# Optimization experiments

Measured on AMD Instinct MI355X. Metric: run time of the kernel, lower is better.

Reference implementation:

```python
import jax, jax.numpy as jnp
import numpy as np

N = 100_000      # nodes
E = 3_200_000    # directed edges
F_IN = 128       # node feature dim
H = 16           # hidden channels


def setup_inputs() -> dict:
    key = jax.random.key(0)
    k0, k1, k2, k3, k4, k5 = jax.random.split(key, 6)
    x = jax.random.normal(k0, (N, F_IN), dtype=jnp.float32)
    edge_index = jax.random.randint(k1, (2, E), 0, N, dtype=jnp.int32)
    W1 = jax.random.normal(k2, (F_IN, H), dtype=jnp.float32) * (1.0 / np.sqrt(F_IN))
    b1 = jax.random.normal(k3, (H,), dtype=jnp.float32) * 0.02
    W2 = jax.random.normal(k4, (H, 1), dtype=jnp.float32) * (1.0 / np.sqrt(H))
    b2 = jax.random.normal(k5, (1,), dtype=jnp.float32) * 0.02
    return {"x": x, "edge_index": edge_index, "W1": W1, "b1": b1, "W2": W2, "b2": b2}


def _gcn_conv(x, src, dst, deg_inv_sqrt, W, b):
    # PyG GCNConv: h = x @ W; out_i = sum_{j->i} norm_ij * h_j + b
    # norm_ij = deg_i^-1/2 * deg_j^-1/2 (degrees include self-loops)
    n = x.shape[0]
    h = x @ W                                   # [N, out]
    norm = deg_inv_sqrt[src] * deg_inv_sqrt[dst]  # [E+N]
    msg = h[src] * norm[:, None]                # gather + scale
    out = jax.ops.segment_sum(msg, dst, num_segments=n)
    return out + b


def reference(x, edge_index, W1, b1, W2, b2):
    n = x.shape[0]
    loops = jnp.arange(n, dtype=edge_index.dtype)
    src = jnp.concatenate([edge_index[0], loops])  # self-loops appended
    dst = jnp.concatenate([edge_index[1], loops])
    # degree of destination nodes (with self-loops), shared by both layers
    deg = jax.ops.segment_sum(jnp.ones_like(dst, dtype=x.dtype), dst, num_segments=n)
    deg_inv_sqrt = jax.lax.rsqrt(jnp.maximum(deg, 1.0))  # deg >= 1 due to self-loops

    h = jax.nn.relu(_gcn_conv(x, src, dst, deg_inv_sqrt, W1, b1))
    out = _gcn_conv(h, src, dst, deg_inv_sqrt, W2, b2)
    return out
```

## Files before the change

kernel.cpp:

```cpp
#include <hip/hip_runtime.h>
#include <hip/hip_fp16.h>

#define FIN 128
#define HC 16
#define NBLK 512
#define NB 391
#define BKT 256
#define SLOT 17408
#define SENT 0xFFFFFFFFu
#define SMAX 5

typedef _Float16 half8 __attribute__((ext_vector_type(8)));
typedef float f32x4 __attribute__((ext_vector_type(4)));

__global__ __launch_bounds__(1024) void count_kernel(const int* __restrict__ dst,
                                                     int* __restrict__ cntTab, int E) {
    __shared__ int cnt[NB];
    int blk = blockIdx.x, t = threadIdx.x;
    for (int i = t; i < NB; i += 1024) cnt[i] = 0;
    __syncthreads();
    int slice = (((E + NBLK - 1) / NBLK) + 3) & ~3;
    int s = blk * slice, e = min(E, s + slice);
    if (s < e) {
        int n4 = (e - s) >> 2;
        const int4* d4 = (const int4*)(dst + s);
        for (int i = t; i < n4; i += 1024) {
            int4 dd = d4[i];
            atomicAdd(&cnt[dd.x >> 8], 1);
            atomicAdd(&cnt[dd.y >> 8], 1);
            atomicAdd(&cnt[dd.z >> 8], 1);
            atomicAdd(&cnt[dd.w >> 8], 1);
        }
    }
    __syncthreads();
    for (int i = t; i < NB; i += 1024) cntTab[i * NBLK + blk] = cnt[i];
}

__global__ void rowscan_kernel(const int* __restrict__ cntTab, int* __restrict__ rowEx,
                               int* __restrict__ bucketTotal) {
    __shared__ int wsum[8];
    int b = blockIdx.x, t = threadIdx.x;
    int own = cntTab[b * NBLK + t];
    int rnd = (own + 15) & ~15;
    int sc = rnd;
#pragma unroll
    for (int off = 1; off < 64; off <<= 1) {
        int v = __shfl_up(sc, off);
        if ((t & 63) >= off) sc += v;
    }
    if ((t & 63) == 63) wsum[t >> 6] = sc;
    __syncthreads();
    int pre = 0;
#pragma unroll
    for (int w = 0; w < 8; ++w)
        if (w < (t >> 6)) pre += wsum[w];
    int inc = sc + pre;
    rowEx[b * NBLK + t] = inc - rnd;
    if (t == NBLK - 1) bucketTotal[b] = inc;
}

__global__ __launch_bounds__(1024) void scatter_kernel(const int* __restrict__ src,
                                                       const int* __restrict__ dst,
                                                       const int* __restrict__ rowEx,
                                                       unsigned int* __restrict__ ebuf, int E) {
    __shared__ int base[NB];
    __shared__ int cur[NB];
    int blk = blockIdx.x, t = threadIdx.x;
    for (int i = t; i < NB; i += 1024) {
        base[i] = i * SLOT + rowEx[i * NBLK + blk];
        cur[i] = 0;
    }
    __syncthreads();
    int slice = (((E + NBLK - 1) / NBLK) + 3) & ~3;
    int s = blk * slice, e = min(E, s + slice);
    if (s < e) {
        int n4 = (e - s) >> 2;
        const int4* d4 = (const int4*)(dst + s);
        const int4* s4 = (const int4*)(src + s);
        for (int i = t; i < n4; i += 1024) {
            int4 dd = d4[i];
            int4 ss = s4[i];
            int b0 = dd.x >> 8, p0 = atomicAdd(&cur[b0], 1);
            ebuf[base[b0] + p0] = ((unsigned)ss.x << 8) | (unsigned)(dd.x & 255);
            int b1 = dd.y >> 8, p1 = atomicAdd(&cur[b1], 1);
            ebuf[base[b1] + p1] = ((unsigned)ss.y << 8) | (unsigned)(dd.y & 255);
            int b2 = dd.z >> 8, p2 = atomicAdd(&cur[b2], 1);
            ebuf[base[b2] + p2] = ((unsigned)ss.z << 8) | (unsigned)(dd.z & 255);
            int b3 = dd.w >> 8, p3 = atomicAdd(&cur[b3], 1);
            ebuf[base[b3] + p3] = ((unsigned)ss.w << 8) | (unsigned)(dd.w & 255);
        }
    }
    __syncthreads();
    for (int i = t; i < NB; i += 1024) {
        int c = cur[i], r = (c + 15) & ~15;
        int bb = base[i];
        for (int p = c; p < r; ++p) ebuf[bb + p] = SENT;
    }
}

__global__ __launch_bounds__(1024) void sortdis_kernel(const unsigned int* __restrict__ ebuf,
                                                       const int* __restrict__ bucketTotal,
                                                       int* __restrict__ csr, int* __restrict__ offs,
                                                       int* __restrict__ deg, float* __restrict__ dis,
                                                       int n) {
    __shared__ int cnt[BKT];
    __shared__ int sc[BKT];
    int b = blockIdx.x, t = threadIdx.x;
    if (t < BKT) cnt[t] = 0;
    __syncthreads();
    int s0 = b * SLOT;
    int total = bucketTotal[b];
    int n4 = total >> 2;
    const uint4* e4 = (const uint4*)(ebuf + s0);
    uint4 ent[SMAX];
    int rk[SMAX][4];
#pragma unroll
    for (int j = 0; j < SMAX; ++j) {
        int idx = j * 1024 + t;
        if (idx < n4) {
            uint4 u = e4[idx];
            ent[j] = u;
            rk[j][0] = (u.x != SENT) ? atomicAdd(&cnt[u.x & 255], 1) : -1;
            rk[j][1] = (u.y != SENT) ? atomicAdd(&cnt[u.y & 255], 1) : -1;
            rk[j][2] = (u.z != SENT) ? atomicAdd(&cnt[u.z & 255], 1) : -1;
            rk[j][3] = (u.w != SENT) ? atomicAdd(&cnt[u.w & 255], 1) : -1;
        } else {
            ent[j].x = SENT; ent[j].y = SENT; ent[j].z = SENT; ent[j].w = SENT;
            rk[j][0] = rk[j][1] = rk[j][2] = rk[j][3] = -1;
        }
    }
    __syncthreads();
    if (t < 64) {
        int c0 = cnt[t * 4], c1 = cnt[t * 4 + 1], c2 = cnt[t * 4 + 2], c3 = cnt[t * 4 + 3];
        int s = c0 + c1 + c2 + c3;
        int scv = s;
#pragma unroll
        for (int off = 1; off < 64; off <<= 1) {
            int v = __shfl_up(scv, off);
            if (t >= off) scv += v;
        }
        int base = scv - s;
        sc[t * 4] = base;
        sc[t * 4 + 1] = base + c0;
        sc[t * 4 + 2] = base + c0 + c1;
        sc[t * 4 + 3] = base + c0 + c1 + c2;
    }
    __syncthreads();
    if (t < BKT) {
        int node = b * BKT + t;
        if (node < n) {
            offs[node] = s0 + sc[t];
            deg[node] = cnt[t];
            dis[node] = rsqrtf((float)cnt[t] + 1.0f);
        }
    }
#pragma unroll
    for (int j = 0; j < SMAX; ++j) {
        unsigned ux = ent[j].x;
        if (ux != SENT) csr[s0 + sc[ux & 255] + rk[j][0]] = (int)(ux >> 8);
        unsigned uy = ent[j].y;
        if (uy != SENT) csr[s0 + sc[uy & 255] + rk[j][1]] = (int)(uy >> 8);
        unsigned uz = ent[j].z;
        if (uz != SENT) csr[s0 + sc[uz & 255] + rk[j][2]] = (int)(uz >> 8);
        unsigned uw = ent[j].w;
        if (uw != SENT) csr[s0 + sc[uw & 255] + rk[j][3]] = (int)(uw >> 8);
    }
}

__global__ void h1_mfma_kernel(const float* __restrict__ x, const float* __restrict__ W1,
                               const float* __restrict__ dis, __half* __restrict__ hs16, int n) {
    __shared__ float xs[64][132];
    int t = threadIdx.x;
    int wave = t >> 6;
    int lane = t & 63;
    int r = lane & 15, g = lane >> 4;
    int rowbase0 = blockIdx.x * 64;
#pragma unroll
    for (int it = 0; it < 8; ++it) {
        int i = it * 256 + t;
        int row = i >> 5, c4 = i & 31;
        int grow = rowbase0 + row;
        const float4* xr = (const float4*)(x + (size_t)(grow < n ? grow : n - 1) * FIN);
        float4 v = xr[c4];
        xs[row][c4 * 4 + 0] = v.x;
        xs[row][c4 * 4 + 1] = v.y;
        xs[row][c4 * 4 + 2] = v.z;
        xs[row][c4 * 4 + 3] = v.w;
    }
    half8 bfrag[4];
#pragma unroll
    for (int i = 0; i < 4; ++i)
#pragma unroll
        for (int j = 0; j < 8; ++j)
            bfrag[i][j] = (_Float16)W1[(i * 32 + g * 8 + j) * HC + r];
    __syncthreads();
    int rowbase = wave * 16;
    f32x4 acc = {0.f, 0.f, 0.f, 0.f};
#pragma unroll
    for (int i = 0; i < 4; ++i) {
        const float4* rowp = (const float4*)&xs[rowbase + r][i * 32 + g * 8];
        float4 v0 = rowp[0];
        float4 v1 = rowp[1];
        half8 afrag;
        afrag[0] = (_Float16)v0.x; afrag[1] = (_Float16)v0.y;
        afrag[2] = (_Float16)v0.z; afrag[3] = (_Float16)v0.w;
        afrag[4] = (_Float16)v1.x; afrag[5] = (_Float16)v1.y;
        afrag[6] = (_Float16)v1.z; afrag[7] = (_Float16)v1.w;
        acc = __builtin_amdgcn_mfma_f32_16x16x32_f16(afrag, bfrag[i], acc, 0, 0, 0);
    }
#pragma unroll
    for (int j = 0; j < 4; ++j) {
        int orow = rowbase0 + rowbase + g * 4 + j;
        if (orow < n) hs16[(size_t)orow * HC + r] = __float2half(acc[j] * dis[orow]);
    }
}

__global__ void pull_layer1_kernel(const int* __restrict__ offs, const int* __restrict__ deg,
                                   const int* __restrict__ csr,
                                   const __half2* __restrict__ hs16, const float* __restrict__ dis,
                                   const float* __restrict__ b1, const float* __restrict__ W2,
                                   float* __restrict__ h2s, int n) {
    int node = (blockIdx.x * blockDim.x + threadIdx.x) >> 6;
    if (node >= n) return;
    int lane = threadIdx.x & 63;
    int cp = lane & 7;
    int eg = lane >> 3;
    int start = offs[node];
    int m = deg[node];
    int sidx = (lane < m) ? csr[start + lane] : 0;
    int mm = min(m, 64);
    float ax = 0.f, ay = 0.f;
    if (mm <= 32) {
#pragma unroll
        for (int t = 0; t < 4; ++t) {
            int e = t * 8 + eg;
            int s = __shfl(sidx, e);
            float2 f = __half22float2(hs16[(size_t)s * 8 + cp]);
            if (e < mm) { ax += f.x; ay += f.y; }
        }
    } else {
#pragma unroll
        for (int t = 0; t < 8; ++t) {
            int e = t * 8 + eg;
            int s = __shfl(sidx, e);
            float2 f = __half22float2(hs16[(size_t)s * 8 + cp]);
            if (e < mm) { ax += f.x; ay += f.y; }
        }
        for (int k = 64 + eg; k < m; k += 8) {
            float2 f = __half22float2(hs16[(size_t)csr[start + k] * 8 + cp]);
            ax += f.x; ay += f.y;
        }
    }
    ax += __shfl_xor(ax, 8);  ay += __shfl_xor(ay, 8);
    ax += __shfl_xor(ax, 16); ay += __shfl_xor(ay, 16);
    ax += __shfl_xor(ax, 32); ay += __shfl_xor(ay, 32);
    float d = dis[node];
    float2 self = __half22float2(hs16[(size_t)node * 8 + cp]);
    float h1a = fmaxf(fmaf(d, ax + self.x, b1[2 * cp]), 0.f);
    float h1b = fmaxf(fmaf(d, ay + self.y, b1[2 * cp + 1]), 0.f);
    float v = h1a * W2[2 * cp] + h1b * W2[2 * cp + 1];
    v += __shfl_xor(v, 1);
    v += __shfl_xor(v, 2);
    v += __shfl_xor(v, 4);
    if (lane == 0) h2s[node] = v * d;
}

__global__ void pull_layer2_kernel(const int* __restrict__ offs, const int* __restrict__ deg,
                                   const int* __restrict__ csr,
                                   const float* __restrict__ h2s, const float* __restrict__ dis,
                                   const float* __restrict__ b2, float* __restrict__ out, int n) {
    int g = blockIdx.x * blockDim.x + threadIdx.x;
    int node = g >> 3;
    if (node >= n) return;
    int q = g & 7;
    int start = offs[node];
    int m = deg[node];
    float a = 0.f;
    int k = q;
    for (; k + 24 < m; k += 32) {
        int i0 = csr[start + k];
        int i1 = csr[start + k + 8];
        int i2 = csr[start + k + 16];
        int i3 = csr[start + k + 24];
        float g0 = h2s[i0], g1 = h2s[i1], g2 = h2s[i2], g3 = h2s[i3];
        a += (g0 + g1) + (g2 + g3);
    }
    for (; k < m; k += 8) a += h2s[csr[start + k]];
    a += __shfl_xor(a, 1);
    a += __shfl_xor(a, 2);
    a += __shfl_xor(a, 4);
    if (q == 0) out[node] = dis[node] * (a + h2s[node]) + b2[0];
}

extern "C" void kernel_launch(void* const* d_in, const int* in_sizes, int n_in,
                              void* d_out, int out_size, void* d_ws, size_t ws_size,
                              hipStream_t stream) {
    const float* x  = (const float*)d_in[0];
    const int* ei   = (const int*)d_in[1];
    const float* W1 = (const float*)d_in[2];
    const float* b1 = (const float*)d_in[3];
    const float* W2 = (const float*)d_in[4];
    const float* b2 = (const float*)d_in[5];
    float* out = (float*)d_out;

    const int n = in_sizes[0] / FIN;
    const int E = in_sizes[1] / 2;
    const int* src = ei;
    const int* dst = ei + E;

    const size_t EB = (size_t)NB * SLOT;
    unsigned int* ebuf = (unsigned int*)d_ws;
    int* csr           = (int*)(ebuf + EB);
    int* cntTab        = csr + EB;
    int* rowEx         = cntTab + NB * NBLK;
    int* bucketTotal   = rowEx + NB * NBLK;
    int* offs          = bucketTotal + NB;
    int* deg           = offs + n;
    float* dis         = (float*)(deg + n);
    float* h2s         = dis + n;
    __half* hs16       = (__half*)ebuf;

    count_kernel<<<NBLK, 1024, 0, stream>>>(dst, cntTab, E);
    rowscan_kernel<<<NB, NBLK, 0, stream>>>(cntTab, rowEx, bucketTotal);
    scatter_kernel<<<NBLK, 1024, 0, stream>>>(src, dst, rowEx, ebuf, E);
    sortdis_kernel<<<NB, 1024, 0, stream>>>(ebuf, bucketTotal, csr, offs, deg, dis, n);
    h1_mfma_kernel<<<(n + 63) / 64, 256, 0, stream>>>(x, W1, dis, hs16, n);
    pull_layer1_kernel<<<(n * 64 + 511) / 512, 512, 0, stream>>>(offs, deg, csr, (const __half2*)hs16, dis, b1, W2, h2s, n);
    pull_layer2_kernel<<<(n * 8 + 255) / 256, 256, 0, stream>>>(offs, deg, csr, h2s, dis, b2, out, n);
}
```

Baseline: 114.1 us.

## Fuse x@W1 MFMA into CSR sort kernel, pack offs/deg, use nontemporal loads

The dense x@W1 MFMA projection now runs inside the per-bucket sort kernel, so each 256-node bucket block computes its own hs16 rows using the locally computed dis values. This removes one launch and the global dis read. Offsets and degrees are packed into a single int2 array, so the pull kernels need one load instead of two. Streaming reads now use nontemporal loads. hs16 moves out of the ebuf alias into its own region. The fused kernel reads x directly from global memory without LDS staging, and adds a sync and register pressure to the 1024-thread sort blocks.

```diff
diff --git a/kernel.cpp b/kernel.cpp
--- a/kernel.cpp
+++ b/kernel.cpp
@@ -12,6 +12,8 @@
 
 typedef _Float16 half8 __attribute__((ext_vector_type(8)));
 typedef float f32x4 __attribute__((ext_vector_type(4)));
+typedef int i32x4 __attribute__((ext_vector_type(4)));
+typedef unsigned int u32x4 __attribute__((ext_vector_type(4)));
 
 __global__ __launch_bounds__(1024) void count_kernel(const int* __restrict__ dst,
                                                      int* __restrict__ cntTab, int E) {
@@ -23,13 +25,13 @@
     int s = blk * slice, e = min(E, s + slice);
     if (s < e) {
         int n4 = (e - s) >> 2;
-        const int4* d4 = (const int4*)(dst + s);
+        const i32x4* d4 = (const i32x4*)(dst + s);
         for (int i = t; i < n4; i += 1024) {
-            int4 dd = d4[i];
-            atomicAdd(&cnt[dd.x >> 8], 1);
-            atomicAdd(&cnt[dd.y >> 8], 1);
-            atomicAdd(&cnt[dd.z >> 8], 1);
-            atomicAdd(&cnt[dd.w >> 8], 1);
+            i32x4 dd = __builtin_nontemporal_load(&d4[i]);
+            atomicAdd(&cnt[dd[0] >> 8], 1);
+            atomicAdd(&cnt[dd[1] >> 8], 1);
+            atomicAdd(&cnt[dd[2] >> 8], 1);
+            atomicAdd(&cnt[dd[3] >> 8], 1);
         }
     }
     __syncthreads();
@@ -75,19 +77,19 @@
     int s = blk * slice, e = min(E, s + slice);
     if (s < e) {
         int n4 = (e - s) >> 2;
-        const int4* d4 = (const int4*)(dst + s);
-        const int4* s4 = (const int4*)(src + s);
+        const i32x4* d4 = (const i32x4*)(dst + s);
+        const i32x4* s4 = (const i32x4*)(src + s);
         for (int i = t; i < n4; i += 1024) {
-            int4 dd = d4[i];
-            int4 ss = s4[i];
-            int b0 = dd.x >> 8, p0 = atomicAdd(&cur[b0], 1);
-            ebuf[base[b0] + p0] = ((unsigned)ss.x << 8) | (unsigned)(dd.x & 255);
-            int b1 = dd.y >> 8, p1 = atomicAdd(&cur[b1], 1);
-            ebuf[base[b1] + p1] = ((unsigned)ss.y << 8) | (unsigned)(dd.y & 255);
-            int b2 = dd.z >> 8, p2 = atomicAdd(&cur[b2], 1);
-            ebuf[base[b2] + p2] = ((unsigned)ss.z << 8) | (unsigned)(dd.z & 255);
-            int b3 = dd.w >> 8, p3 = atomicAdd(&cur[b3], 1);
-            ebuf[base[b3] + p3] = ((unsigned)ss.w << 8) | (unsigned)(dd.w & 255);
+            i32x4 dd = __builtin_nontemporal_load(&d4[i]);
+            i32x4 ss = __builtin_nontemporal_load(&s4[i]);
+            int b0 = dd[0] >> 8, p0 = atomicAdd(&cur[b0], 1);
+            ebuf[base[b0] + p0] = ((unsigned)ss[0] << 8) | (unsigned)(dd[0] & 255);
+            int b1 = dd[1] >> 8, p1 = atomicAdd(&cur[b1], 1);
+            ebuf[base[b1] + p1] = ((unsigned)ss[1] << 8) | (unsigned)(dd[1] & 255);
+            int b2 = dd[2] >> 8, p2 = atomicAdd(&cur[b2], 1);
+            ebuf[base[b2] + p2] = ((unsigned)ss[2] << 8) | (unsigned)(dd[2] & 255);
+            int b3 = dd[3] >> 8, p3 = atomicAdd(&cur[b3], 1);
+            ebuf[base[b3] + p3] = ((unsigned)ss[3] << 8) | (unsigned)(dd[3] & 255);
         }
     }
     __syncthreads();
@@ -98,34 +100,35 @@
     }
 }
 
-__global__ __launch_bounds__(1024) void sortdis_kernel(const unsigned int* __restrict__ ebuf,
-                                                       const int* __restrict__ bucketTotal,
-                                                       int* __restrict__ csr, int* __restrict__ offs,
-                                                       int* __restrict__ deg, float* __restrict__ dis,
-                                                       int n) {
+__global__ __launch_bounds__(1024) void sortdis_h1_kernel(
+    const unsigned int* __restrict__ ebuf, const int* __restrict__ bucketTotal,
+    const float* __restrict__ x, const float* __restrict__ W1,
+    int* __restrict__ csr, int2* __restrict__ od, float* __restrict__ dis,
+    __half* __restrict__ hs16, int n) {
     __shared__ int cnt[BKT];
     __shared__ int sc[BKT];
+    __shared__ float disL[BKT];
     int b = blockIdx.x, t = threadIdx.x;
     if (t < BKT) cnt[t] = 0;
     __syncthreads();
     int s0 = b * SLOT;
     int total = bucketTotal[b];
     int n4 = total >> 2;
-    const uint4* e4 = (const uint4*)(ebuf + s0);
-    uint4 ent[SMAX];
+    const u32x4* e4 = (const u32x4*)(ebuf + s0);
+    u32x4 ent[SMAX];
     int rk[SMAX][4];
 #pragma unroll
     for (int j = 0; j < SMAX; ++j) {
         int idx = j * 1024 + t;
         if (idx < n4) {
-            uint4 u = e4[idx];
+            u32x4 u = __builtin_nontemporal_load(&e4[idx]);
             ent[j] = u;
-            rk[j][0] = (u.x != SENT) ? atomicAdd(&cnt[u.x & 255], 1) : -1;
-            rk[j][1] = (u.y != SENT) ? atomicAdd(&cnt[u.y & 255], 1) : -1;
-            rk[j][2] = (u.z != SENT) ? atomicAdd(&cnt[u.z & 255], 1) : -1;
-            rk[j][3] = (u.w != SENT) ? atomicAdd(&cnt[u.w & 255], 1) : -1;
+            rk[j][0] = (u[0] != SENT) ? atomicAdd(&cnt[u[0] & 255], 1) : -1;
+            rk[j][1] = (u[1] != SENT) ? atomicAdd(&cnt[u[1] & 255], 1) : -1;
+            rk[j][2] = (u[2] != SENT) ? atomicAdd(&cnt[u[2] & 255], 1) : -1;
+            rk[j][3] = (u[3] != SENT) ? atomicAdd(&cnt[u[3] & 255], 1) : -1;
         } else {
-            ent[j].x = SENT; ent[j].y = SENT; ent[j].z = SENT; ent[j].w = SENT;
+            ent[j][0] = SENT; ent[j][1] = SENT; ent[j][2] = SENT; ent[j][3] = SENT;
             rk[j][0] = rk[j][1] = rk[j][2] = rk[j][3] = -1;
         }
     }
@@ -148,75 +151,58 @@
     __syncthreads();
     if (t < BKT) {
         int node = b * BKT + t;
+        float dv = rsqrtf((float)cnt[t] + 1.0f);
+        disL[t] = dv;
         if (node < n) {
-            offs[node] = s0 + sc[t];
-            deg[node] = cnt[t];
-            dis[node] = rsqrtf((float)cnt[t] + 1.0f);
+            od[node] = make_int2(s0 + sc[t], cnt[t]);
+            dis[node] = dv;
         }
     }
 #pragma unroll
     for (int j = 0; j < SMAX; ++j) {
-        unsigned ux = ent[j].x;
+        unsigned ux = ent[j][0];
         if (ux != SENT) csr[s0 + sc[ux & 255] + rk[j][0]] = (int)(ux >> 8);
-        unsigned uy = ent[j].y;
+        unsigned uy = ent[j][1];
         if (uy != SENT) csr[s0 + sc[uy & 255] + rk[j][1]] = (int)(uy >> 8);
-        unsigned uz = ent[j].z;
+        unsigned uz = ent[j][2];
         if (uz != SENT) csr[s0 + sc[uz & 255] + rk[j][2]] = (int)(uz >> 8);
-        unsigned uw = ent[j].w;
+        unsigned uw = ent[j][3];
         if (uw != SENT) csr[s0 + sc[uw & 255] + rk[j][3]] = (int)(uw >> 8);
     }
-}
-
-__global__ void h1_mfma_kernel(const float* __restrict__ x, const float* __restrict__ W1,
-                               const float* __restrict__ dis, __half* __restrict__ hs16, int n) {
-    __shared__ float xs[64][132];
-    int t = threadIdx.x;
-    int wave = t >> 6;
-    int lane = t & 63;
+    __syncthreads();
+    int wave = t >> 6, lane = t & 63;
     int r = lane & 15, g = lane >> 4;
-    int rowbase0 = blockIdx.x * 64;
-#pragma unroll
-    for (int it = 0; it < 8; ++it) {
-        int i = it * 256 + t;
-        int row = i >> 5, c4 = i & 31;
-        int grow = rowbase0 + row;
-        const float4* xr = (const float4*)(x + (size_t)(grow < n ? grow : n - 1) * FIN);
-        float4 v = xr[c4];
-        xs[row][c4 * 4 + 0] = v.x;
-        xs[row][c4 * 4 + 1] = v.y;
-        xs[row][c4 * 4 + 2] = v.z;
-        xs[row][c4 * 4 + 3] = v.w;
-    }
     half8 bfrag[4];
 #pragma unroll
     for (int i = 0; i < 4; ++i)
 #pragma unroll
         for (int j = 0; j < 8; ++j)
             bfrag[i][j] = (_Float16)W1[(i * 32 + g * 8 + j) * HC + r];
-    __syncthreads();
-    int rowbase = wave * 16;
+    int lrow = wave * 16;
+    int grow = b * BKT + lrow + r;
+    const f32x4* xr = (const f32x4*)(x + (size_t)(grow < n ? grow : n - 1) * FIN);
     f32x4 acc = {0.f, 0.f, 0.f, 0.f};
 #pragma unroll
     for (int i = 0; i < 4; ++i) {
-        const float4* rowp = (const float4*)&xs[rowbase + r][i * 32 + g * 8];
-        float4 v0 = rowp[0];
-        float4 v1 = rowp[1];
+        int idx = i * 8 + g * 2;
+        f32x4 v0 = __builtin_nontemporal_load(&xr[idx]);
+        f32x4 v1 = __builtin_nontemporal_load(&xr[idx + 1]);
         half8 afrag;
-        afrag[0] = (_Float16)v0.x; afrag[1] = (_Float16)v0.y;
-        afrag[2] = (_Float16)v0.z; afrag[3] = (_Float16)v0.w;
-        afrag[4] = (_Float16)v1.x; afrag[5] = (_Float16)v1.y;
-        afrag[6] = (_Float16)v1.z; afrag[7] = (_Float16)v1.w;
+        afrag[0] = (_Float16)v0[0]; afrag[1] = (_Float16)v0[1];
+        afrag[2] = (_Float16)v0[2]; afrag[3] = (_Float16)v0[3];
+        afrag[4] = (_Float16)v1[0]; afrag[5] = (_Float16)v1[1];
+        afrag[6] = (_Float16)v1[2]; afrag[7] = (_Float16)v1[3];
         acc = __builtin_amdgcn_mfma_f32_16x16x32_f16(afrag, bfrag[i], acc, 0, 0, 0);
     }
 #pragma unroll
     for (int j = 0; j < 4; ++j) {
-        int orow = rowbase0 + rowbase + g * 4 + j;
-        if (orow < n) hs16[(size_t)orow * HC + r] = __float2half(acc[j] * dis[orow]);
-    }
-}
-
-__global__ void pull_layer1_kernel(const int* __restrict__ offs, const int* __restrict__ deg,
-                                   const int* __restrict__ csr,
+        int lr = lrow + g * 4 + j;
+        int orow = b * BKT + lr;
+        if (orow < n) hs16[(size_t)orow * HC + r] = __float2half(acc[j] * disL[lr]);
+    }
+}
+
+__global__ void pull_layer1_kernel(const int2* __restrict__ od, const int* __restrict__ csr,
                                    const __half2* __restrict__ hs16, const float* __restrict__ dis,
                                    const float* __restrict__ b1, const float* __restrict__ W2,
                                    float* __restrict__ h2s, int n) {
@@ -225,9 +211,9 @@
     int lane = threadIdx.x & 63;
     int cp = lane & 7;
     int eg = lane >> 3;
-    int start = offs[node];
-    int m = deg[node];
-    int sidx = (lane < m) ? csr[start + lane] : 0;
+    int2 v2 = od[node];
+    int start = v2.x, m = v2.y;
+    int sidx = (lane < m) ? __builtin_nontemporal_load(&csr[start + lane]) : 0;
     int mm = min(m, 64);
     float ax = 0.f, ay = 0.f;
     if (mm <= 32) {
@@ -265,27 +251,26 @@
     if (lane == 0) h2s[node] = v * d;
 }
 
-__global__ void pull_layer2_kernel(const int* __restrict__ offs, const int* __restrict__ deg,
-                                   const int* __restrict__ csr,
+__global__ void pull_layer2_kernel(const int2* __restrict__ od, const int* __restrict__ csr,
                                    const float* __restrict__ h2s, const float* __restrict__ dis,
                                    const float* __restrict__ b2, float* __restrict__ out, int n) {
     int g = blockIdx.x * blockDim.x + threadIdx.x;
     int node = g >> 3;
     if (node >= n) return;
     int q = g & 7;
-    int start = offs[node];
-    int m = deg[node];
+    int2 v2 = od[node];
+    int start = v2.x, m = v2.y;
     float a = 0.f;
     int k = q;
     for (; k + 24 < m; k += 32) {
-        int i0 = csr[start + k];
-        int i1 = csr[start + k + 8];
-        int i2 = csr[start + k + 16];
-        int i3 = csr[start + k + 24];
+        int i0 = __builtin_nontemporal_load(&csr[start + k]);
+        int i1 = __builtin_nontemporal_load(&csr[start + k + 8]);
+        int i2 = __builtin_nontemporal_load(&csr[start + k + 16]);
+        int i3 = __builtin_nontemporal_load(&csr[start + k + 24]);
         float g0 = h2s[i0], g1 = h2s[i1], g2 = h2s[i2], g3 = h2s[i3];
         a += (g0 + g1) + (g2 + g3);
     }
-    for (; k < m; k += 8) a += h2s[csr[start + k]];
+    for (; k < m; k += 8) a += h2s[__builtin_nontemporal_load(&csr[start + k])];
     a += __shfl_xor(a, 1);
     a += __shfl_xor(a, 2);
     a += __shfl_xor(a, 4);
@@ -314,17 +299,15 @@
     int* cntTab        = csr + EB;
     int* rowEx         = cntTab + NB * NBLK;
     int* bucketTotal   = rowEx + NB * NBLK;
-    int* offs          = bucketTotal + NB;
-    int* deg           = offs + n;
-    float* dis         = (float*)(deg + n);
+    int2* od           = (int2*)(bucketTotal + 392);
+    float* dis         = (float*)(od + n);
     float* h2s         = dis + n;
-    __half* hs16       = (__half*)ebuf;
+    __half* hs16       = (__half*)(h2s + n);
 
     count_kernel<<<NBLK, 1024, 0, stream>>>(dst, cntTab, E);
     rowscan_kernel<<<NB, NBLK, 0, stream>>>(cntTab, rowEx, bucketTotal);
     scatter_kernel<<<NBLK, 1024, 0, stream>>>(src, dst, rowEx, ebuf, E);
-    sortdis_kernel<<<NB, 1024, 0, stream>>>(ebuf, bucketTotal, csr, offs, deg, dis, n);
-    h1_mfma_kernel<<<(n + 63) / 64, 256, 0, stream>>>(x, W1, dis, hs16, n);
-    pull_layer1_kernel<<<(n * 64 + 511) / 512, 512, 0, stream>>>(offs, deg, csr, (const __half2*)hs16, dis, b1, W2, h2s, n);
-    pull_layer2_kernel<<<(n * 8 + 255) / 256, 256, 0, stream>>>(offs, deg, csr, h2s, dis, b2, out, n);
-}
+    sortdis_h1_kernel<<<NB, 1024, 0, stream>>>(ebuf, bucketTotal, x, W1, csr, od, dis, hs16, n);
+    pull_layer1_kernel<<<(n * 64 + 511) / 512, 512, 0, stream>>>(od, csr, (const __half2*)hs16, dis, b1, W2, h2s, n);
+    pull_layer2_kernel<<<(n * 8 + 255) / 256, 256, 0, stream>>>(od, csr, h2s, dis, b2, out, n);
+}
```

After: 134.1 us. 1.17x slower.
